# Performance work log

Measured on AMD Instinct MI355X. Metric: run time of the kernel, lower is better.

The kernel has to match this reference:

```python
import jax, jax.numpy as jnp
import numpy as np

B, N, T, H = 128, 16, 200, 64
NEG = -(2.0 ** 32) + 1.0

def setup_inputs() -> dict:
    key = jax.random.key(0)
    ks = jax.random.split(key, 10)
    queries = jax.random.normal(ks[0], (B, N, H), dtype=jnp.float32)
    keys = jax.random.normal(ks[1], (B, T, H), dtype=jnp.float32)
    keys_length = jax.random.randint(ks[2], (B,), 1, T + 1)
    # MLP params: Linear(4H->80), Linear(80->40), Linear(40->1); stored as [in,out]
    W1 = jax.random.normal(ks[3], (4 * H, 80), dtype=jnp.float32) * (1.0 / np.sqrt(4 * H))
    b1 = jnp.zeros((80,), dtype=jnp.float32)
    W2 = jax.random.normal(ks[4], (80, 40), dtype=jnp.float32) * (1.0 / np.sqrt(80))
    b2 = jnp.zeros((40,), dtype=jnp.float32)
    W3 = jax.random.normal(ks[5], (40, 1), dtype=jnp.float32) * (1.0 / np.sqrt(40))
    b3 = jnp.zeros((1,), dtype=jnp.float32)
    return {"queries": queries, "keys": keys, "keys_length": keys_length,
            "W1": W1, "b1": b1, "W2": W2, "b2": b2, "W3": W3, "b3": b3}

def reference(queries, keys, keys_length, W1, b1, W2, b2, W3, b3):
    b, n, h = queries.shape
    t = keys.shape[1]
    q = queries[:, :, None, :]                      # [B,N,1,H]
    k = keys[:, None, :, :]                         # [B,1,T,H]
    qb = jnp.broadcast_to(q, (b, n, t, h))
    kb = jnp.broadcast_to(k, (b, n, t, h))
    feat = jnp.concatenate([qb, kb, qb - kb, qb * kb], axis=-1)  # [B,N,T,4H]
    x = jax.nn.sigmoid(feat @ W1 + b1)
    x = jax.nn.sigmoid(x @ W2 + b2)
    s = (x @ W3 + b3)[..., 0]                       # [B,N,T]
    mask = jnp.arange(t)[None, :] < keys_length[:, None]  # [B,T]
    s = jnp.where(mask[:, None, :], s, NEG)
    s = s / jnp.sqrt(jnp.float32(h))
    w = jax.nn.softmax(s, axis=-1)                  # [B,N,T]
    out = jnp.einsum('bnt,bth->bnh', w, keys)       # [B,N,H]
    return out
```

## Files before the change

### kernel.cpp

```cpp
#include <hip/hip_runtime.h>
#include <hip/hip_bf16.h>
#include <math.h>

#define B_  128
#define N_  16
#define T_  200
#define H_  64
#define J1  80
#define J2  40
#define NTILE 13
#define NEGV -4294967295.0f

typedef __attribute__((ext_vector_type(8))) short bf16x8;
typedef __attribute__((ext_vector_type(4))) float f32x4;

__device__ __forceinline__ float sigmoidf_(float x) {
    return __builtin_amdgcn_rcpf(1.0f + __expf(-x));
}
__device__ __forceinline__ short f2b(float x) {
    unsigned u = __float_as_uint(x);
    return (short)((u + 0x7FFF + ((u >> 16) & 1)) >> 16);
}
__device__ __forceinline__ unsigned pack2(float a, float b) {
    return (unsigned)(unsigned short)f2b(a) | ((unsigned)(unsigned short)f2b(b) << 16);
}
__device__ __forceinline__ unsigned cvtpk(float a, float b) {
    unsigned r;
    asm("v_cvt_pk_bf16_f32 %0, %1, %2" : "=v"(r) : "v"(a), "v"(b));
    return r;
}
__device__ __forceinline__ unsigned kqword(unsigned w, float ql, float qh) {
    float lo = __uint_as_float(w << 16) * ql;
    float hi = __uint_as_float(w & 0xffff0000u) * qh;
    return cvtpk(lo, hi);
}

#define P_QW 160
#define P_WB 20
#define P_KB 416
#define P_W2 9
#define P_PB 1
__global__ void prep(const float* __restrict__ queries,
                     const float* __restrict__ keys,
                     const float* __restrict__ W1,
                     const float* __restrict__ b1,
                     const float* __restrict__ W2,
                     const float* __restrict__ b2,
                     const float* __restrict__ W3,
                     float* __restrict__ QW,
                     unsigned* __restrict__ WBFu,
                     bf16x8* __restrict__ kbf0, bf16x8* __restrict__ kbf1,
                     unsigned* __restrict__ W2F,
                     float* __restrict__ b2p, float* __restrict__ W3p) {
    const int blk = blockIdx.x, tid = threadIdx.x;
    if (blk < P_QW) {
        int idx = blk * 256 + tid;
        int bn = idx / 20, j = (idx % 20) * 4;
        float4 acc = *(const float4*)(b1 + j);
        const float* qp = queries + bn * H_;
        for (int h = 0; h < H_; ++h) {
            float qh = qp[h];
            float4 wa = *(const float4*)(W1 + h * J1 + j);
            float4 wc = *(const float4*)(W1 + (128 + h) * J1 + j);
            acc.x = fmaf(qh, wa.x + wc.x, acc.x);
            acc.y = fmaf(qh, wa.y + wc.y, acc.y);
            acc.z = fmaf(qh, wa.z + wc.z, acc.z);
            acc.w = fmaf(qh, wa.w + wc.w, acc.w);
        }
        *(float4*)(QW + bn * J1 + j) = acc;
    } else if (blk < P_QW + P_WB) {
        int idx = (blk - P_QW) * 256 + tid;
        int rp = idx & 3, l = (idx >> 2) & 63, fi = idx >> 8;
        int j  = (fi % 5) * 16 + (l & 15);
        int R  = (fi / 5) * 32 + 8 * (l >> 4) + 2 * rp;
        float a, b;
        if (R < 64) {
            a = W1[(192 + R) * J1 + j];
            b = W1[(193 + R) * J1 + j];
        } else {
            int r2 = R - 64;
            a = W1[(64 + r2) * J1 + j] - W1[(128 + r2) * J1 + j];
            b = W1[(65 + r2) * J1 + j] - W1[(129 + r2) * J1 + j];
        }
        WBFu[idx] = pack2(a, b);
    } else if (blk < P_QW + P_WB + P_KB) {
        int idx = (blk - P_QW - P_WB) * 256 + tid;
        int l  = idx & 63, bm = idx >> 6;
        int mt = bm % NTILE, b = bm / NTILE;
        int t  = mt * 16 + (l & 15); if (t > T_ - 1) t = T_ - 1;
        int rg = l >> 4;
        const float* kr = keys + ((size_t)(b * T_ + t)) * H_ + 8 * rg;
        float4 a0 = *(const float4*)(kr);
        float4 a1 = *(const float4*)(kr + 4);
        float4 a2 = *(const float4*)(kr + 32);
        float4 a3 = *(const float4*)(kr + 36);
        bf16x8 f0, f1;
        f0[0] = f2b(a0.x); f0[1] = f2b(a0.y); f0[2] = f2b(a0.z); f0[3] = f2b(a0.w);
        f0[4] = f2b(a1.x); f0[5] = f2b(a1.y); f0[6] = f2b(a1.z); f0[7] = f2b(a1.w);
        f1[0] = f2b(a2.x); f1[1] = f2b(a2.y); f1[2] = f2b(a2.z); f1[3] = f2b(a2.w);
        f1[4] = f2b(a3.x); f1[5] = f2b(a3.y); f1[6] = f2b(a3.z); f1[7] = f2b(a3.w);
        kbf0[idx] = f0; kbf1[idx] = f1;
    } else if (blk < P_QW + P_WB + P_KB + P_W2) {
        int idx = (blk - P_QW - P_WB - P_KB) * 256 + tid;
        if (idx < 9 * 64 * 4) {
            int rp = idx & 3;
            int l  = (idx >> 2) & 63;
            int f  = idx >> 8;
            int m  = (f / 3) * 16 + (l & 15);
            int k0 = (f % 3) * 32 + 8 * (l >> 4) + 2 * rp;
            float a = (k0     < J1 && m < J2) ? W2[k0 * J2 + m]       : 0.0f;
            float b = (k0 + 1 < J1 && m < J2) ? W2[(k0 + 1) * J2 + m] : 0.0f;
            W2F[idx] = pack2(a, b);
        }
    } else {
        if (tid < 48) {
            b2p[tid] = (tid < J2) ? b2[tid] : 0.0f;
            W3p[tid] = (tid < J2) ? W3[tid] : 0.0f;
        }
    }
}

__global__ __launch_bounds__(512, 4) void attn_w2(
        const float* __restrict__ queries, const float* __restrict__ keys,
        const int*   __restrict__ keys_length,
        const float* __restrict__ QW,
        const bf16x8* __restrict__ kbf0, const bf16x8* __restrict__ kbf1,
        const bf16x8* __restrict__ WALL,
        const float* __restrict__ b2p, const float* __restrict__ W3p,
        const float* __restrict__ b3,
        float* __restrict__ out) {
    const int tid  = threadIdx.x;
    const int lane = tid & 63, wv = tid >> 6;
    const int blk  = (blockIdx.x & 7) * 64 + (blockIdx.x >> 3);
    const int bnL  = wv >> 1;
    const int half = wv & 1;
    const int bn   = blk * 4 + bnL;
    const int b    = bn >> 4;
    const int cl   = lane & 15, rg = lane >> 4;

    __shared__ __align__(16) short wlds[29 * 64 * 8];
    __shared__ __align__(16) short X1[8][16][108];
    __shared__ float z3s[4][208];
    __shared__ float wsm[4][208];
    __shared__ float part[8][64];

    for (int i = tid; i < 29 * 64; i += 512)
        ((bf16x8*)wlds)[i] = WALL[i];
    #pragma unroll
    for (int i = 0; i < 4; ++i)
        X1[wv][rg + 4 * i][80 + cl] = 0;
    __syncthreads();

    const bf16x8* wl = (const bf16x8*)wlds;

    const float* qp = queries + bn * H_;
    float4 qa = *(const float4*)(qp + 8 * rg);
    float4 qb = *(const float4*)(qp + 8 * rg + 4);
    float4 qc = *(const float4*)(qp + 32 + 8 * rg);
    float4 qd = *(const float4*)(qp + 36 + 8 * rg);
    float4 qw4[5];
    #pragma unroll
    for (int nt = 0; nt < 5; ++nt)
        qw4[nt] = *(const float4*)(QW + bn * J1 + 16 * nt + 4 * rg);
    float4 b24[3], w34[3];
    #pragma unroll
    for (int nt = 0; nt < 3; ++nt) {
        b24[nt] = *(const float4*)(b2p + 16 * nt + 4 * rg);
        w34[nt] = *(const float4*)(W3p + 16 * nt + 4 * rg);
    }
    const float b3v = b3[0];
    const float* kb = keys + (size_t)b * T_ * H_;

    const int mt0 = half * 7;
    const int mtE = half ? NTILE : 7;
    bf16x8 nk0 = kbf0[(b * NTILE + mt0) * 64 + lane];
    bf16x8 nk1 = kbf1[(b * NTILE + mt0) * 64 + lane];
    #pragma unroll 1
    for (int mt = mt0; mt < mtE; ++mt) {
        bf16x8 k0 = nk0, k1 = nk1;
        {
            int mn = mt + 1 < mtE ? mt + 1 : mtE - 1;
            nk0 = kbf0[(b * NTILE + mn) * 64 + lane];
            nk1 = kbf1[(b * NTILE + mn) * 64 + lane];
        }
        const uint4 kw0 = *(const uint4*)&k0;
        const uint4 kw1 = *(const uint4*)&k1;
        uint4 kqw0, kqw1;
        kqw0.x = kqword(kw0.x, qa.x, qa.y);
        kqw0.y = kqword(kw0.y, qa.z, qa.w);
        kqw0.z = kqword(kw0.z, qb.x, qb.y);
        kqw0.w = kqword(kw0.w, qb.z, qb.w);
        kqw1.x = kqword(kw1.x, qc.x, qc.y);
        kqw1.y = kqword(kw1.y, qc.z, qc.w);
        kqw1.z = kqword(kw1.z, qd.x, qd.y);
        kqw1.w = kqword(kw1.w, qd.z, qd.w);
        bf16x8 kq0 = *(bf16x8*)&kqw0;
        bf16x8 kq1 = *(bf16x8*)&kqw1;

        f32x4 acc[5];
        #pragma unroll
        for (int nt = 0; nt < 5; ++nt) {
            acc[nt][0] = qw4[nt].x; acc[nt][1] = qw4[nt].y;
            acc[nt][2] = qw4[nt].z; acc[nt][3] = qw4[nt].w;
        }
        #pragma unroll
        for (int nt = 0; nt < 5; ++nt) {
            acc[nt] = __builtin_amdgcn_mfma_f32_16x16x32_bf16(wl[( 0 + nt) * 64 + lane], kq0, acc[nt], 0, 0, 0);
            acc[nt] = __builtin_amdgcn_mfma_f32_16x16x32_bf16(wl[( 5 + nt) * 64 + lane], kq1, acc[nt], 0, 0, 0);
            acc[nt] = __builtin_amdgcn_mfma_f32_16x16x32_bf16(wl[(10 + nt) * 64 + lane], k0,  acc[nt], 0, 0, 0);
            acc[nt] = __builtin_amdgcn_mfma_f32_16x16x32_bf16(wl[(15 + nt) * 64 + lane], k1,  acc[nt], 0, 0, 0);
        }

        #pragma unroll
        for (int nt = 0; nt < 5; ++nt) {
            unsigned r0 = cvtpk(sigmoidf_(acc[nt][0]), sigmoidf_(acc[nt][1]));
            unsigned r1 = cvtpk(sigmoidf_(acc[nt][2]), sigmoidf_(acc[nt][3]));
            *(uint2*)&X1[wv][cl][16 * nt + 4 * rg] = make_uint2(r0, r1);
        }

        f32x4 acc2[3];
        #pragma unroll
        for (int nt = 0; nt < 3; ++nt) {
            acc2[nt][0] = b24[nt].x; acc2[nt][1] = b24[nt].y;
            acc2[nt][2] = b24[nt].z; acc2[nt][3] = b24[nt].w;
        }
        #pragma unroll
        for (int ks = 0; ks < 3; ++ks) {
            bf16x8 xa = *(const bf16x8*)&X1[wv][cl][8 * rg + 32 * ks];
            acc2[0] = __builtin_amdgcn_mfma_f32_16x16x32_bf16(wl[(20 + 0 + ks) * 64 + lane], xa, acc2[0], 0, 0, 0);
            acc2[1] = __builtin_amdgcn_mfma_f32_16x16x32_bf16(wl[(20 + 3 + ks) * 64 + lane], xa, acc2[1], 0, 0, 0);
            acc2[2] = __builtin_amdgcn_mfma_f32_16x16x32_bf16(wl[(20 + 6 + ks) * 64 + lane], xa, acc2[2], 0, 0, 0);
        }

        float p = 0.f;
        #pragma unroll
        for (int nt = 0; nt < 3; ++nt) {
            p = fmaf(sigmoidf_(acc2[nt][0]), w34[nt].x, p);
            p = fmaf(sigmoidf_(acc2[nt][1]), w34[nt].y, p);
            p = fmaf(sigmoidf_(acc2[nt][2]), w34[nt].z, p);
            p = fmaf(sigmoidf_(acc2[nt][3]), w34[nt].w, p);
        }
        p += __shfl_xor(p, 16);
        p += __shfl_xor(p, 32);
        if (rg == 0) z3s[bnL][mt * 16 + cl] = p + b3v;
    }
    __syncthreads();

    const int L  = keys_length[b];
    const int t0 = lane, t1 = lane + 64, t2 = lane + 128, t3 = lane + 192;
    float r0 = z3s[bnL][t0], r1 = z3s[bnL][t1], r2 = z3s[bnL][t2];
    float r3 = (t3 < 208) ? z3s[bnL][t3] : 0.0f;
    float s0 = (t0 < L) ? r0 * 0.125f : NEGV * 0.125f;
    float s1 = (t1 < L) ? r1 * 0.125f : NEGV * 0.125f;
    float s2 = (t2 < L) ? r2 * 0.125f : NEGV * 0.125f;
    float s3 = (t3 < T_ && t3 < L) ? r3 * 0.125f : ((t3 < T_) ? NEGV * 0.125f : -3.0e38f);

    float mx = fmaxf(fmaxf(s0, s1), fmaxf(s2, s3));
    #pragma unroll
    for (int off = 32; off > 0; off >>= 1) mx = fmaxf(mx, __shfl_xor(mx, off));

    float e0 = __expf(s0 - mx);
    float e1 = __expf(s1 - mx);
    float e2 = __expf(s2 - mx);
    float e3 = (t3 < T_) ? __expf(s3 - mx) : 0.0f;
    float sm = e0 + e1 + e2 + e3;
    #pragma unroll
    for (int off = 32; off > 0; off >>= 1) sm += __shfl_xor(sm, off);

    float inv = __builtin_amdgcn_rcpf(sm);
    wsm[bnL][t0] = e0 * inv;
    wsm[bnL][t1] = e1 * inv;
    wsm[bnL][t2] = e2 * inv;
    if (t3 < T_) wsm[bnL][t3] = e3 * inv;
    __syncthreads();

    float acc_ = 0.f;
    {
        int tb = 100 * half;
        #pragma unroll 10
        for (int t = tb; t < tb + 100; ++t)
            acc_ = fmaf(wsm[bnL][t], kb[(size_t)t * H_ + lane], acc_);
    }
    part[wv][lane] = acc_;
    __syncthreads();
    if (half == 0)
        out[bn * H_ + lane] = part[wv][lane] + part[wv + 1][lane];
}

__global__ __launch_bounds__(256, 3) void attn_nows(
        const float* __restrict__ queries, const float* __restrict__ keys,
        const int*   __restrict__ keys_length,
        const float* __restrict__ W1, const float* __restrict__ b1,
        const float* __restrict__ W2, const float* __restrict__ b2,
        const float* __restrict__ W3, const float* __restrict__ b3,
        float* __restrict__ out) {
    const int tid = threadIdx.x;
    const int bn = (blockIdx.x & 7) * 256 + (blockIdx.x >> 3);
    const int b  = bn >> 4;

    __shared__ float kT[H_][T_ + 1];
    __shared__ float wsm[T_];
    __shared__ float part[256];
    __shared__ float red[8];
    __shared__ float QWq[J1];

    for (int idx = tid; idx < T_ * H_; idx += 256) {
        int t = idx >> 6, h = idx & 63;
        kT[h][t] = keys[(b * T_ + t) * H_ + h];
    }
    if (tid < J1) {
        float acc = b1[tid];
        const float* qp = queries + bn * H_;
        for (int h = 0; h < H_; ++h)
            acc = fmaf(qp[h], W1[h * J1 + tid] + W1[(128 + h) * J1 + tid], acc);
        QWq[tid] = acc;
    }
    __syncthreads();

    const int tt = (tid < T_) ? tid : 0;
    const float* qp = queries + bn * H_;

    float qk[H_];
    #pragma unroll
    for (int h = 0; h < H_; ++h) qk[h] = qp[h] * kT[h][tt];

    float z2[J2];
    #pragma unroll
    for (int m = 0; m < J2; ++m) z2[m] = b2[m];

    #pragma unroll 1
    for (int c = 0; c < 4; ++c) {
        const int j0 = c * 20;
        float z1c[20];
        #pragma unroll
        for (int j = 0; j < 20; ++j) z1c[j] = QWq[j0 + j];
        #pragma unroll
        for (int h = 0; h < H_; ++h) {
            float kh = kT[h][tt];
            const float* Wd = W1 + (192 + h) * J1 + j0;
            const float* Wb = W1 + (64 + h) * J1 + j0;
            const float* Wc = W1 + (128 + h) * J1 + j0;
            #pragma unroll
            for (int j = 0; j < 20; ++j)
                z1c[j] = fmaf(qk[h], Wd[j], fmaf(kh, Wb[j] - Wc[j], z1c[j]));
        }
        #pragma unroll
        for (int j = 0; j < 20; ++j) {
            float x = sigmoidf_(z1c[j]);
            const float* w2 = W2 + (j0 + j) * J2;
            #pragma unroll
            for (int m = 0; m < J2; ++m) z2[m] = fmaf(x, w2[m], z2[m]);
        }
    }

    float z3 = b3[0];
    #pragma unroll
    for (int m = 0; m < J2; ++m) z3 = fmaf(sigmoidf_(z2[m]), W3[m], z3);

    const int L = keys_length[b];
    float s = (tid < T_) ? ((tid < L) ? z3 : NEGV) * 0.125f : -3.0e38f;

    float mx = s;
    #pragma unroll
    for (int off = 32; off > 0; off >>= 1) mx = fmaxf(mx, __shfl_xor(mx, off));
    if ((tid & 63) == 0) red[tid >> 6] = mx;
    __syncthreads();
    mx = fmaxf(fmaxf(red[0], red[1]), fmaxf(red[2], red[3]));

    float e = (tid < T_) ? __expf(s - mx) : 0.0f;
    float sm = e;
    #pragma unroll
    for (int off = 32; off > 0; off >>= 1) sm += __shfl_xor(sm, off);
    __syncthreads();
    if ((tid & 63) == 0) red[4 + (tid >> 6)] = sm;
    __syncthreads();
    sm = red[4] + red[5] + red[6] + red[7];

    if (tid < T_) wsm[tid] = e / sm;
    __syncthreads();

    {
        int h = tid & 63, p = tid >> 6;
        float acc = 0.f;
        int t0 = p * 50;
        for (int t = t0; t < t0 + 50; ++t)
            acc = fmaf(wsm[t], kT[h][t], acc);
        part[tid] = acc;
    }
    __syncthreads();
    if (tid < 64) {
        out[bn * H_ + tid] = part[tid] + part[64 + tid] + part[128 + tid] + part[192 + tid];
    }
}

extern "C" void kernel_launch(void* const* d_in, const int* in_sizes, int n_in,
                              void* d_out, int out_size, void* d_ws, size_t ws_size,
                              hipStream_t stream) {
    const float* queries = (const float*)d_in[0];
    const float* keys    = (const float*)d_in[1];
    const int*   klen    = (const int*)  d_in[2];
    const float* W1 = (const float*)d_in[3];
    const float* b1 = (const float*)d_in[4];
    const float* W2 = (const float*)d_in[5];
    const float* b2 = (const float*)d_in[6];
    const float* W3 = (const float*)d_in[7];
    const float* b3 = (const float*)d_in[8];
    float* out = (float*)d_out;

    const size_t nkbf = (size_t)B_ * NTILE * 64;
    const size_t need = 655360 + 2 * 1703936 + 20480 + 9216 + 512;

    if (ws_size >= need) {
        char* base = (char*)d_ws;
        float*  QW   = (float*)base;
        bf16x8* kbf0 = (bf16x8*)(base + 655360);
        bf16x8* kbf1 = kbf0 + nkbf;
        bf16x8* WBF  = kbf1 + nkbf;
        unsigned* W2F = (unsigned*)((char*)WBF + 20480);
        float*  b2p  = (float*)((char*)W2F + 9216);
        float*  W3p  = b2p + 64;

        prep<<<dim3(P_QW + P_WB + P_KB + P_W2 + P_PB), dim3(256), 0, stream>>>(
            queries, keys, W1, b1, W2, b2, W3,
            QW, (unsigned*)WBF, kbf0, kbf1, W2F, b2p, W3p);
        attn_w2<<<dim3(512), dim3(512), 0, stream>>>(
            queries, keys, klen, QW, kbf0, kbf1, WBF, b2p, W3p, b3, out);
    } else {
        attn_nows<<<dim3(B_ * N_), dim3(256), 0, stream>>>(
            queries, keys, klen, W1, b1, W2, b2, W3, b3, out);
    }
}
```

Baseline: 39.72 us.

## Fold query into per-row W1 weights, halving layer-1 MFMAs per tile

Rewrites the layer-1 product so the q*k and (q-k) terms are folded into a per-query weight matrix q∘W1d + (W1b−W1c), built in shared memory once per block. Each key tile then needs only two MFMAs per output tile instead of four, and the per-tile k*q bf16 conversion is removed. Blocks shrink to 256 threads covering 2 queries, the grid doubles to 1024, and W2 fragments are now read from global memory instead of LDS. The cost is a per-block setup step and extra bf16 rounding of the folded weights.

```diff
diff --git a/kernel.cpp b/kernel.cpp
--- a/kernel.cpp
+++ b/kernel.cpp
@@ -29,14 +29,9 @@
     asm("v_cvt_pk_bf16_f32 %0, %1, %2" : "=v"(r) : "v"(a), "v"(b));
     return r;
 }
-__device__ __forceinline__ unsigned kqword(unsigned w, float ql, float qh) {
-    float lo = __uint_as_float(w << 16) * ql;
-    float hi = __uint_as_float(w & 0xffff0000u) * qh;
-    return cvtpk(lo, hi);
-}
 
 #define P_QW 160
-#define P_WB 20
+#define P_WB 10
 #define P_KB 416
 #define P_W2 9
 #define P_PB 1
@@ -48,7 +43,7 @@
                      const float* __restrict__ b2,
                      const float* __restrict__ W3,
                      float* __restrict__ QW,
-                     unsigned* __restrict__ WBFu,
+                     float* __restrict__ w1df, float* __restrict__ wbcf,
                      bf16x8* __restrict__ kbf0, bf16x8* __restrict__ kbf1,
                      unsigned* __restrict__ W2F,
                      float* __restrict__ b2p, float* __restrict__ W3p) {
@@ -70,19 +65,14 @@
         *(float4*)(QW + bn * J1 + j) = acc;
     } else if (blk < P_QW + P_WB) {
         int idx = (blk - P_QW) * 256 + tid;
-        int rp = idx & 3, l = (idx >> 2) & 63, fi = idx >> 8;
-        int j  = (fi % 5) * 16 + (l & 15);
-        int R  = (fi / 5) * 32 + 8 * (l >> 4) + 2 * rp;
-        float a, b;
-        if (R < 64) {
-            a = W1[(192 + R) * J1 + j];
-            b = W1[(193 + R) * J1 + j];
-        } else {
-            int r2 = R - 64;
-            a = W1[(64 + r2) * J1 + j] - W1[(128 + r2) * J1 + j];
-            b = W1[(65 + r2) * J1 + j] - W1[(129 + r2) * J1 + j];
-        }
-        WBFu[idx] = pack2(a, b);
+        int rp = idx & 3, l = (idx >> 2) & 63, f = idx >> 8;
+        int j  = (f % 5) * 16 + (l & 15);
+        int R  = (f / 5) * 32 + 8 * (l >> 4) + 2 * rp;
+        int o  = (f * 64 + l) * 8 + 2 * rp;
+        w1df[o]     = W1[(192 + R) * J1 + j];
+        w1df[o + 1] = W1[(193 + R) * J1 + j];
+        wbcf[o]     = W1[(64 + R) * J1 + j] - W1[(128 + R) * J1 + j];
+        wbcf[o + 1] = W1[(65 + R) * J1 + j] - W1[(129 + R) * J1 + j];
     } else if (blk < P_QW + P_WB + P_KB) {
         int idx = (blk - P_QW - P_WB) * 256 + tid;
         int l  = idx & 63, bm = idx >> 6;
@@ -120,44 +110,57 @@
     }
 }
 
-__global__ __launch_bounds__(512, 4) void attn_w2(
+__global__ __launch_bounds__(256, 4) void attn_bl(
         const float* __restrict__ queries, const float* __restrict__ keys,
         const int*   __restrict__ keys_length,
         const float* __restrict__ QW,
         const bf16x8* __restrict__ kbf0, const bf16x8* __restrict__ kbf1,
-        const bf16x8* __restrict__ WALL,
+        const float* __restrict__ w1df, const float* __restrict__ wbcf,
+        const bf16x8* __restrict__ W2F,
         const float* __restrict__ b2p, const float* __restrict__ W3p,
         const float* __restrict__ b3,
         float* __restrict__ out) {
     const int tid  = threadIdx.x;
     const int lane = tid & 63, wv = tid >> 6;
-    const int blk  = (blockIdx.x & 7) * 64 + (blockIdx.x >> 3);
+    const int blk  = (blockIdx.x & 7) * 128 + (blockIdx.x >> 3);
     const int bnL  = wv >> 1;
     const int half = wv & 1;
-    const int bn   = blk * 4 + bnL;
+    const int bn   = blk * 2 + bnL;
     const int b    = bn >> 4;
     const int cl   = lane & 15, rg = lane >> 4;
 
-    __shared__ __align__(16) short wlds[29 * 64 * 8];
-    __shared__ __align__(16) short X1[8][16][108];
-    __shared__ float z3s[4][208];
-    __shared__ float wsm[4][208];
-    __shared__ float part[8][64];
-
-    for (int i = tid; i < 29 * 64; i += 512)
-        ((bf16x8*)wlds)[i] = WALL[i];
+    __shared__ __align__(16) short BnL[2][10 * 64 * 8];
+    __shared__ __align__(16) short X1[4][16][108];
+    __shared__ float z3s[2][208];
+    __shared__ float wsm[2][208];
+    __shared__ float part[4][64];
+
+    {
+        const float* qpz = queries + bn * H_ + half * 32 + rg * 8;
+        float4 q0 = *(const float4*)(qpz);
+        float4 q1 = *(const float4*)(qpz + 4);
+        #pragma unroll
+        for (int ff = 0; ff < 5; ++ff) {
+            const int f = 5 * half + ff;
+            const float* wp = w1df + (f * 64 + lane) * 8;
+            const float* cp = wbcf + (f * 64 + lane) * 8;
+            float4 wA = *(const float4*)(wp);
+            float4 wB = *(const float4*)(wp + 4);
+            float4 cA = *(const float4*)(cp);
+            float4 cB = *(const float4*)(cp + 4);
+            uint4 o;
+            o.x = cvtpk(fmaf(q0.x, wA.x, cA.x), fmaf(q0.y, wA.y, cA.y));
+            o.y = cvtpk(fmaf(q0.z, wA.z, cA.z), fmaf(q0.w, wA.w, cA.w));
+            o.z = cvtpk(fmaf(q1.x, wB.x, cB.x), fmaf(q1.y, wB.y, cB.y));
+            o.w = cvtpk(fmaf(q1.z, wB.z, cB.z), fmaf(q1.w, wB.w, cB.w));
+            *(uint4*)&BnL[bnL][(f * 64 + lane) * 8] = o;
+        }
+    }
     #pragma unroll
     for (int i = 0; i < 4; ++i)
         X1[wv][rg + 4 * i][80 + cl] = 0;
     __syncthreads();
 
-    const bf16x8* wl = (const bf16x8*)wlds;
-
-    const float* qp = queries + bn * H_;
-    float4 qa = *(const float4*)(qp + 8 * rg);
-    float4 qb = *(const float4*)(qp + 8 * rg + 4);
-    float4 qc = *(const float4*)(qp + 32 + 8 * rg);
-    float4 qd = *(const float4*)(qp + 36 + 8 * rg);
     float4 qw4[5];
     #pragma unroll
     for (int nt = 0; nt < 5; ++nt)
@@ -183,19 +186,6 @@
             nk0 = kbf0[(b * NTILE + mn) * 64 + lane];
             nk1 = kbf1[(b * NTILE + mn) * 64 + lane];
         }
-        const uint4 kw0 = *(const uint4*)&k0;
-        const uint4 kw1 = *(const uint4*)&k1;
-        uint4 kqw0, kqw1;
-        kqw0.x = kqword(kw0.x, qa.x, qa.y);
-        kqw0.y = kqword(kw0.y, qa.z, qa.w);
-        kqw0.z = kqword(kw0.z, qb.x, qb.y);
-        kqw0.w = kqword(kw0.w, qb.z, qb.w);
-        kqw1.x = kqword(kw1.x, qc.x, qc.y);
-        kqw1.y = kqword(kw1.y, qc.z, qc.w);
-        kqw1.z = kqword(kw1.z, qd.x, qd.y);
-        kqw1.w = kqword(kw1.w, qd.z, qd.w);
-        bf16x8 kq0 = *(bf16x8*)&kqw0;
-        bf16x8 kq1 = *(bf16x8*)&kqw1;
 
         f32x4 acc[5];
         #pragma unroll
@@ -205,10 +195,10 @@
         }
         #pragma unroll
         for (int nt = 0; nt < 5; ++nt) {
-            acc[nt] = __builtin_amdgcn_mfma_f32_16x16x32_bf16(wl[( 0 + nt) * 64 + lane], kq0, acc[nt], 0, 0, 0);
-            acc[nt] = __builtin_amdgcn_mfma_f32_16x16x32_bf16(wl[( 5 + nt) * 64 + lane], kq1, acc[nt], 0, 0, 0);
-            acc[nt] = __builtin_amdgcn_mfma_f32_16x16x32_bf16(wl[(10 + nt) * 64 + lane], k0,  acc[nt], 0, 0, 0);
-            acc[nt] = __builtin_amdgcn_mfma_f32_16x16x32_bf16(wl[(15 + nt) * 64 + lane], k1,  acc[nt], 0, 0, 0);
+            bf16x8 a0 = *(const bf16x8*)&BnL[bnL][((0 + nt) * 64 + lane) * 8];
+            bf16x8 a1 = *(const bf16x8*)&BnL[bnL][((5 + nt) * 64 + lane) * 8];
+            acc[nt] = __builtin_amdgcn_mfma_f32_16x16x32_bf16(a0, k0, acc[nt], 0, 0, 0);
+            acc[nt] = __builtin_amdgcn_mfma_f32_16x16x32_bf16(a1, k1, acc[nt], 0, 0, 0);
         }
 
         #pragma unroll
@@ -227,9 +217,12 @@
         #pragma unroll
         for (int ks = 0; ks < 3; ++ks) {
             bf16x8 xa = *(const bf16x8*)&X1[wv][cl][8 * rg + 32 * ks];
-            acc2[0] = __builtin_amdgcn_mfma_f32_16x16x32_bf16(wl[(20 + 0 + ks) * 64 + lane], xa, acc2[0], 0, 0, 0);
-            acc2[1] = __builtin_amdgcn_mfma_f32_16x16x32_bf16(wl[(20 + 3 + ks) * 64 + lane], xa, acc2[1], 0, 0, 0);
-            acc2[2] = __builtin_amdgcn_mfma_f32_16x16x32_bf16(wl[(20 + 6 + ks) * 64 + lane], xa, acc2[2], 0, 0, 0);
+            bf16x8 w0 = W2F[(0 + ks) * 64 + lane];
+            bf16x8 w1 = W2F[(3 + ks) * 64 + lane];
+            bf16x8 w2 = W2F[(6 + ks) * 64 + lane];
+            acc2[0] = __builtin_amdgcn_mfma_f32_16x16x32_bf16(w0, xa, acc2[0], 0, 0, 0);
+            acc2[1] = __builtin_amdgcn_mfma_f32_16x16x32_bf16(w1, xa, acc2[1], 0, 0, 0);
+            acc2[2] = __builtin_amdgcn_mfma_f32_16x16x32_bf16(w2, xa, acc2[2], 0, 0, 0);
         }
 
         float p = 0.f;
@@ -408,23 +401,25 @@
     float* out = (float*)d_out;
 
     const size_t nkbf = (size_t)B_ * NTILE * 64;
-    const size_t need = 655360 + 2 * 1703936 + 20480 + 9216 + 512;
+    const size_t need = 655360 + 2 * 1703936 + 2 * 20480 + 9216 + 512;
 
     if (ws_size >= need) {
         char* base = (char*)d_ws;
         float*  QW   = (float*)base;
         bf16x8* kbf0 = (bf16x8*)(base + 655360);
         bf16x8* kbf1 = kbf0 + nkbf;
-        bf16x8* WBF  = kbf1 + nkbf;
-        unsigned* W2F = (unsigned*)((char*)WBF + 20480);
+        float*  w1df = (float*)(kbf1 + nkbf);
+        float*  wbcf = w1df + 5120;
+        unsigned* W2F = (unsigned*)(wbcf + 5120);
         float*  b2p  = (float*)((char*)W2F + 9216);
         float*  W3p  = b2p + 64;
 
         prep<<<dim3(P_QW + P_WB + P_KB + P_W2 + P_PB), dim3(256), 0, stream>>>(
             queries, keys, W1, b1, W2, b2, W3,
-            QW, (unsigned*)WBF, kbf0, kbf1, W2F, b2p, W3p);
-        attn_w2<<<dim3(512), dim3(512), 0, stream>>>(
-            queries, keys, klen, QW, kbf0, kbf1, WBF, b2p, W3p, b3, out);
+            QW, w1df, wbcf, kbf0, kbf1, W2F, b2p, W3p);
+        attn_bl<<<dim3(1024), dim3(256), 0, stream>>>(
+            queries, keys, klen, QW, kbf0, kbf1, w1df, wbcf,
+            (const bf16x8*)W2F, b2p, W3p, b3, out);
     } else {
         attn_nows<<<dim3(B_ * N_), dim3(256), 0, stream>>>(
             queries, keys, klen, W1, b1, W2, b2, W3, b3, out);
```

Measured after the change: 53.28 us. 34.1% more time.
